# Kernel optimization log

Measured on AMD Instinct MI355X. Metric: run time of the kernel, lower is better.

The kernel has to match this reference:

```python
import jax, jax.numpy as jnp
import numpy as np

D_MODEL = 1024
N_HEADS = 16
HEAD_DIM = D_MODEL // N_HEADS
D_FF = 4096
B, S = 2, 2048
EPS = 1e-6
NEG = -1e9


def setup_inputs() -> dict:
    key = jax.random.key(0)
    ks = jax.random.split(key, 16)
    sd = 1.0 / np.sqrt(D_MODEL)
    sf = 1.0 / np.sqrt(D_FF)
    inp = {
        "x": jax.random.normal(ks[0], (B, S, D_MODEL), jnp.float32),
        # causal mask, broadcastable over batch and heads
        "mask": jnp.tril(jnp.ones((S, S), jnp.bool_))[None, None, :, :],
        # attention projections, torch Linear layout [out, in]
        "Wq": jax.random.normal(ks[1], (D_MODEL, D_MODEL), jnp.float32) * sd,
        "bq": jnp.zeros((D_MODEL,), jnp.float32),
        "Wk": jax.random.normal(ks[2], (D_MODEL, D_MODEL), jnp.float32) * sd,
        "bk": jnp.zeros((D_MODEL,), jnp.float32),
        "Wv": jax.random.normal(ks[3], (D_MODEL, D_MODEL), jnp.float32) * sd,
        "bv": jnp.zeros((D_MODEL,), jnp.float32),
        "Wo": jax.random.normal(ks[4], (D_MODEL, D_MODEL), jnp.float32) * sd,
        "bo": jnp.zeros((D_MODEL,), jnp.float32),
        # layer norms
        "ln1_g": jnp.ones((D_MODEL,), jnp.float32),
        "ln1_b": jnp.zeros((D_MODEL,), jnp.float32),
        "ln2_g": jnp.ones((D_MODEL,), jnp.float32),
        "ln2_b": jnp.zeros((D_MODEL,), jnp.float32),
        # FFN
        "W1": jax.random.normal(ks[5], (D_FF, D_MODEL), jnp.float32) * sd,
        "b1": jnp.zeros((D_FF,), jnp.float32),
        "W2": jax.random.normal(ks[6], (D_MODEL, D_FF), jnp.float32) * sf,
        "b2": jnp.zeros((D_MODEL,), jnp.float32),
    }
    return inp


def _layer_norm(x, g, b):
    mu = jnp.mean(x, axis=-1, keepdims=True)
    var = jnp.var(x, axis=-1, keepdims=True)
    return (x - mu) * jax.lax.rsqrt(var + EPS) * g + b


def _linear(x, W, b):
    return jnp.einsum('...i,oi->...o', x, W) + b


def _attention(x, mask, Wq, bq, Wk, bk, Wv, bv, Wo, bo):
    Bsz, Sq, _ = x.shape
    q = _linear(x, Wq, bq).reshape(Bsz, Sq, N_HEADS, HEAD_DIM)
    k = _linear(x, Wk, bk).reshape(Bsz, Sq, N_HEADS, HEAD_DIM)
    v = _linear(x, Wv, bv).reshape(Bsz, Sq, N_HEADS, HEAD_DIM)
    # [B,H,S,S]
    scores = jnp.einsum('bqhd,bkhd->bhqk', q, k) / np.sqrt(HEAD_DIM)
    scores = jnp.where(mask, scores, NEG)
    weights = jax.nn.softmax(scores, axis=-1)
    ctx = jnp.einsum('bhqk,bkhd->bqhd', weights, v).reshape(Bsz, Sq, D_MODEL)
    return _linear(ctx, Wo, bo)


def reference(x, mask, Wq, bq, Wk, bk, Wv, bv, Wo, bo,
              ln1_g, ln1_b, ln2_g, ln2_b, W1, b1, W2, b2):
    # pre-LN attention block (dropout = identity at inference)
    h = _layer_norm(x, ln1_g, ln1_b)
    x = x + _attention(h, mask, Wq, bq, Wk, bk, Wv, bv, Wo, bo)
    # pre-LN FFN block
    h = _layer_norm(x, ln2_g, ln2_b)
    h = jax.nn.gelu(_linear(h, W1, b1), approximate=False)
    x = x + _linear(h, W2, b2)
    return x
```

## Files before the change

kernel.cpp:

```cpp
#include <hip/hip_runtime.h>
#include <hip/hip_bf16.h>
#include <cstdint>
#include <cstddef>

typedef unsigned short u16;
typedef __bf16 bf16x8 __attribute__((ext_vector_type(8)));
typedef float f32x4 __attribute__((ext_vector_type(4)));

#define D_MODEL 1024
#define D_FF    4096
#define BATCH   2
#define SEQ     2048
#define NH      16
#define HD      64
#define ROWS    (BATCH*SEQ)
#define QKVS    3072

__device__ __forceinline__ u16 f2bf(float f) {
    union { float f; uint32_t u; } v; v.f = f;
    uint32_t u = v.u;
    u += 0x7FFF + ((u >> 16) & 1);
    return (u16)(u >> 16);
}

__device__ __forceinline__ uint32_t cvtpk_bf16(float lo, float hi) {
    uint32_t r;
    asm("v_cvt_pk_bf16_f32 %0, %1, %2" : "=v"(r) : "v"(lo), "v"(hi));
    return r;
}

__device__ __forceinline__ bf16x8 ldg8(const u16* p) {
    return *reinterpret_cast<const bf16x8*>(p);
}

__device__ __forceinline__ f32x4 mfma16(bf16x8 a, bf16x8 b, f32x4 c) {
    return __builtin_amdgcn_mfma_f32_16x16x32_bf16(a, b, c, 0, 0, 0);
}

__device__ __forceinline__ void gld_lds16(const void* g, void* l) {
    __builtin_amdgcn_global_load_lds(
        (const __attribute__((address_space(1))) void*)g,
        (__attribute__((address_space(3))) void*)l, 16, 0, 0);
}

__device__ __forceinline__ float gelu_f(float x) {
    float u = fmaf(0.044715f * x, x * x, x);
    float z = fminf(-2.3022036f * u, 126.0f);
    float e = __builtin_amdgcn_exp2f(z);
    return x / (1.0f + e);
}

struct alignas(8) U16x4 { u16 x, y, z, w; };

__global__ void cvt_all(const float* __restrict__ s0, const float* __restrict__ s1,
                        const float* __restrict__ s2, const float* __restrict__ s3,
                        const float* __restrict__ s4, const float* __restrict__ s5,
                        u16* __restrict__ out)
{
    const size_t MM1 = 1 << 20;
    size_t i = ((size_t)blockIdx.x * 256 + threadIdx.x) * 4;
    const float* src; size_t off;
    if      (i <     MM1) { src = s0; off = i; }
    else if (i < 2 * MM1) { src = s1; off = i - MM1; }
    else if (i < 3 * MM1) { src = s2; off = i - 2 * MM1; }
    else if (i < 4 * MM1) { src = s3; off = i - 3 * MM1; }
    else if (i < 8 * MM1) { src = s4; off = i - 4 * MM1; }
    else                  { src = s5; off = i - 8 * MM1; }
    float4 f = *reinterpret_cast<const float4*>(src + off);
    U16x4 o{ f2bf(f.x), f2bf(f.y), f2bf(f.z), f2bf(f.w) };
    *reinterpret_cast<U16x4*>(out + i) = o;
}

__global__ __launch_bounds__(256) void ln_bf16(
    const float* __restrict__ x, const float* __restrict__ g,
    const float* __restrict__ b, u16* __restrict__ out)
{
    int row = blockIdx.x;
    const float* xr = x + (size_t)row * D_MODEL;
    int t = threadIdx.x;
    float4 v = *reinterpret_cast<const float4*>(xr + t * 4);
    float s = v.x + v.y + v.z + v.w;
    float q = v.x*v.x + v.y*v.y + v.z*v.z + v.w*v.w;
    #pragma unroll
    for (int off = 1; off < 64; off <<= 1) {
        s += __shfl_xor(s, off);
        q += __shfl_xor(q, off);
    }
    __shared__ float red[8];
    if ((t & 63) == 0) { red[(t >> 6) * 2] = s; red[(t >> 6) * 2 + 1] = q; }
    __syncthreads();
    float sum = red[0] + red[2] + red[4] + red[6];
    float sq  = red[1] + red[3] + red[5] + red[7];
    float mu  = sum * (1.0f / D_MODEL);
    float var = sq * (1.0f / D_MODEL) - mu * mu;
    float rstd = rsqrtf(var + 1e-6f);
    float4 gg = *reinterpret_cast<const float4*>(g + t * 4);
    float4 bb = *reinterpret_cast<const float4*>(b + t * 4);
    U16x4 o{ f2bf((v.x - mu) * rstd * gg.x + bb.x),
             f2bf((v.y - mu) * rstd * gg.y + bb.y),
             f2bf((v.z - mu) * rstd * gg.z + bb.z),
             f2bf((v.w - mu) * rstd * gg.w + bb.w) };
    *reinterpret_cast<U16x4*>(out + (size_t)row * D_MODEL + t * 4) = o;
}

#define EPI_BF16   0
#define EPI_RESF32 1
#define EPI_GELU   2
#define EPI_PART   3

template<int EPI>
__global__ __launch_bounds__(512, 1) void gemm256(
    const u16* __restrict__ A, const u16* __restrict__ B,
    const float* __restrict__ bias, const float* __restrict__ res,
    u16* __restrict__ outb, float* __restrict__ outf,
    int M, int N, int K)
{
    __shared__ u16 As[2][256 * 64];
    __shared__ u16 Bs[2][256 * 64];
    const int t = threadIdx.x;
    const int lane = t & 63, w = t >> 6;
    const int lr = lane & 15, lg = lane >> 4;
    const int wr = w >> 2, wc = w & 3;

    const int gw  = N >> 8;
    const int nwg = gridDim.x;
    const int cpx = nwg >> 3;
    const int swz = ((int)blockIdx.x & 7) * cpx + ((int)blockIdx.x >> 3);
    const int by = swz / gw, bx = swz % gw;
    const int brow = by * 256, bcol = bx * 256;

    const u16* Ag = A + (size_t)brow * K;
    const u16* Bg = B + (size_t)bcol * K;

    f32x4 acc[8][4] = {};
    const int NT = K >> 6;

    auto stageAll = [&](int buf, int kt) {
        #pragma unroll
        for (int c = 0; c < 8; ++c) {
            const u16* g = (c < 4) ? Ag : Bg;
            u16* l = (c < 4) ? As[buf] : Bs[buf];
            int cc = c & 3;
            int row = cc * 64 + (t >> 3);
            int sg = (t & 7) ^ (row & 7);
            gld_lds16(g + (size_t)row * K + kt * 64 + sg * 8, l + cc * 4096 + t * 8);
        }
    };

    auto computeTile = [&](int buf) {
        const u16* la = As[buf];
        const u16* lb = Bs[buf];
        bf16x8 breg[4][2];
        #pragma unroll
        for (int ni = 0; ni < 4; ++ni) {
            int row = wc * 64 + ni * 16 + lr;
            const u16* bp = lb + row * 64;
            int key = row & 7;
            breg[ni][0] = ldg8(bp + ((0 + lg) ^ key) * 8);
            breg[ni][1] = ldg8(bp + ((4 + lg) ^ key) * 8);
        }
        #pragma unroll
        for (int mi = 0; mi < 8; ++mi) {
            int row = wr * 128 + mi * 16 + lr;
            const u16* ap = la + row * 64;
            int key = row & 7;
            bf16x8 a0 = ldg8(ap + ((0 + lg) ^ key) * 8);
            bf16x8 a1 = ldg8(ap + ((4 + lg) ^ key) * 8);
            __builtin_amdgcn_s_setprio(1);
            #pragma unroll
            for (int ni = 0; ni < 4; ++ni) {
                acc[mi][ni] = mfma16(a0, breg[ni][0], acc[mi][ni]);
                acc[mi][ni] = mfma16(a1, breg[ni][1], acc[mi][ni]);
            }
            __builtin_amdgcn_s_setprio(0);
        }
    };

    stageAll(0, 0);
    stageAll(1, 1);
    asm volatile("s_waitcnt vmcnt(8)" ::: "memory");
    __builtin_amdgcn_s_barrier();

    for (int kt = 0; kt < NT; ++kt) {
        computeTile(kt & 1);
        if (kt + 1 == NT) break;
        __builtin_amdgcn_s_barrier();
        if (kt + 2 < NT) {
            stageAll(kt & 1, kt + 2);
            asm volatile("s_waitcnt vmcnt(8)" ::: "memory");
        } else {
            asm volatile("s_waitcnt vmcnt(0)" ::: "memory");
        }
        __builtin_amdgcn_s_barrier();
    }

    #pragma unroll
    for (int mi = 0; mi < 8; ++mi) {
        int r0 = brow + wr * 128 + mi * 16 + lg * 4;
        #pragma unroll
        for (int ni = 0; ni < 4; ++ni) {
            int c = bcol + wc * 64 + ni * 16 + lr;
            float bv = bias[c];
            #pragma unroll
            for (int j = 0; j < 4; ++j) {
                float v = acc[mi][ni][j] + bv;
                size_t idx = (size_t)(r0 + j) * N + c;
                if constexpr (EPI == EPI_GELU) {
                    outb[idx] = f2bf(gelu_f(v));
                } else if constexpr (EPI == EPI_RESF32) {
                    outf[idx] = v + res[idx];
                } else {
                    outb[idx] = f2bf(v);
                }
            }
        }
    }
}

template<int EPI>
__global__ __launch_bounds__(256, 2) void gemm_bt(
    const u16* __restrict__ A, const u16* __restrict__ B,
    const float* __restrict__ bias, const float* __restrict__ res,
    u16* __restrict__ outb, float* __restrict__ outf,
    int M, int N, int K, int KS)
{
    __shared__ u16 As[2][128 * 64];
    __shared__ u16 Bs[2][128 * 64];
    const int t = threadIdx.x;
    const int lane = t & 63;
    const int w = t >> 6;
    const int lr = lane & 15, lg = lane >> 4;
    const int wrr = (w >> 1) * 64, wcc = (w & 1) * 64;
    const int brow = blockIdx.y * 128, bcol = blockIdx.x * 128;
    const int kz = blockIdx.z;
    const u16* Ag = A + (size_t)brow * KS + (size_t)kz * K;
    const u16* Bg = B + (size_t)bcol * KS + (size_t)kz * K;

    f32x4 acc[4][4] = {};

    const int NT = K >> 6;

    auto stage = [&](int buf, int kt) {
        const u16* ga = Ag + kt * 64;
        const u16* gb = Bg + kt * 64;
        u16* la = As[buf];
        u16* lb = Bs[buf];
        #pragma unroll
        for (int c = 0; c < 4; ++c) {
            int f = c * 256 + t;
            int row = f >> 3, slot = f & 7;
            int sg = slot ^ (row & 7);
            gld_lds16(ga + (size_t)row * KS + sg * 8, la + f * 8);
            gld_lds16(gb + (size_t)row * KS + sg * 8, lb + f * 8);
        }
    };

    auto compute = [&](int buf) {
        const u16* la = As[buf];
        const u16* lb = Bs[buf];
        bf16x8 af[4][2];
        #pragma unroll
        for (int mi = 0; mi < 4; ++mi) {
            int row = wrr + mi * 16 + lr;
            int base = row * 64;
            af[mi][0] = *reinterpret_cast<const bf16x8*>(la + base + ((0 + lg) ^ (row & 7)) * 8);
            af[mi][1] = *reinterpret_cast<const bf16x8*>(la + base + ((4 + lg) ^ (row & 7)) * 8);
        }
        __builtin_amdgcn_s_setprio(1);
        #pragma unroll
        for (int ni = 0; ni < 4; ++ni) {
            int row = wcc + ni * 16 + lr;
            int base = row * 64;
            bf16x8 b0 = *reinterpret_cast<const bf16x8*>(lb + base + ((0 + lg) ^ (row & 7)) * 8);
            bf16x8 b1 = *reinterpret_cast<const bf16x8*>(lb + base + ((4 + lg) ^ (row & 7)) * 8);
            #pragma unroll
            for (int mi = 0; mi < 4; ++mi) {
                acc[mi][ni] = mfma16(af[mi][0], b0, acc[mi][ni]);
                acc[mi][ni] = mfma16(af[mi][1], b1, acc[mi][ni]);
            }
        }
        __builtin_amdgcn_s_setprio(0);
    };

    stage(0, 0);
    if (NT > 1) {
        stage(1, 1);
        asm volatile("s_waitcnt vmcnt(8)" ::: "memory");
    } else {
        asm volatile("s_waitcnt vmcnt(0)" ::: "memory");
    }
    __builtin_amdgcn_s_barrier();

    for (int kt = 0; kt < NT; ++kt) {
        compute(kt & 1);
        if (kt + 1 == NT) break;
        __builtin_amdgcn_s_barrier();
        if (kt + 2 < NT) {
            stage(kt & 1, kt + 2);
            asm volatile("s_waitcnt vmcnt(8)" ::: "memory");
        } else {
            asm volatile("s_waitcnt vmcnt(0)" ::: "memory");
        }
        __builtin_amdgcn_s_barrier();
    }

    #pragma unroll
    for (int mi = 0; mi < 4; ++mi) {
        int r0 = brow + wrr + mi * 16 + lg * 4;
        #pragma unroll
        for (int ni = 0; ni < 4; ++ni) {
            int c = bcol + wcc + ni * 16 + lr;
            float bv = 0.f;
            if constexpr (EPI != EPI_PART) bv = bias[c];
            #pragma unroll
            for (int j = 0; j < 4; ++j) {
                float v = acc[mi][ni][j] + bv;
                size_t idx = (size_t)(r0 + j) * N + c;
                if constexpr (EPI == EPI_GELU) {
                    outb[idx] = f2bf(gelu_f(v));
                } else if constexpr (EPI == EPI_RESF32) {
                    outf[idx] = v + res[idx];
                } else if constexpr (EPI == EPI_PART) {
                    outf[idx + (size_t)kz * M * N] = v;
                } else {
                    outb[idx] = f2bf(v);
                }
            }
        }
    }
}

__global__ void ffn2_reduce(const float* __restrict__ p,
                            const float* __restrict__ b2,
                            const float* __restrict__ x2,
                            float* __restrict__ out)
{
    size_t i = ((size_t)blockIdx.x * 256 + threadIdx.x) * 4;
    float4 a0 = *reinterpret_cast<const float4*>(p + i);
    float4 a1 = *reinterpret_cast<const float4*>(p + (size_t)ROWS * D_MODEL + i);
    float4 r  = *reinterpret_cast<const float4*>(x2 + i);
    float4 bb = *reinterpret_cast<const float4*>(b2 + (i & (D_MODEL - 1)));
    float4 o;
    o.x = a0.x + a1.x + r.x + bb.x;
    o.y = a0.y + a1.y + r.y + bb.y;
    o.z = a0.z + a1.z + r.z + bb.z;
    o.w = a0.w + a1.w + r.w + bb.w;
    *reinterpret_cast<float4*>(out + i) = o;
}

__global__ __launch_bounds__(256) void vtrans(
    const u16* __restrict__ QKV, u16* __restrict__ VT)
{
    __shared__ u16 tile[64][72];
    const int st = blockIdx.x * 64;
    const int bh = blockIdx.y;
    const int b = bh >> 4, h = bh & 15;
    const int t = threadIdx.x;

    #pragma unroll
    for (int c = 0; c < 2; ++c) {
        int tok = c * 32 + (t >> 3);
        int d0 = (t & 7) * 8;
        bf16x8 v = ldg8(QKV + ((size_t)(b * SEQ + st + tok)) * QKVS + 2048 + h * HD + d0);
        *reinterpret_cast<bf16x8*>(&tile[tok][d0]) = v;
    }
    __syncthreads();
    u16* dst = VT + (size_t)bh * HD * SEQ + st;
    #pragma unroll
    for (int c = 0; c < 2; ++c) {
        int d = c * 32 + (t >> 3);
        int tok0 = (t & 7) * 8;
        u16 vals[8];
        #pragma unroll
        for (int i = 0; i < 8; ++i) vals[i] = tile[tok0 + i][d];
        *reinterpret_cast<bf16x8*>(dst + (size_t)d * SEQ + tok0) =
            *reinterpret_cast<const bf16x8*>(vals);
    }
}

#define QBLK  64
#define KVBLK 64

__global__ __launch_bounds__(256, 3) void attn7(
    const u16* __restrict__ QKV, const u16* __restrict__ VT,
    u16* __restrict__ O)
{
    __shared__ u16 Ks[2][64 * 64];
    __shared__ u16 Vs[2][64 * 64];
    __shared__ u16 Pl[4][16 * 72];

    const int i  = blockIdx.x;
    const int bh = blockIdx.y;
    const int b = bh >> 4, h = bh & 15;
    const int qta = 31 - i;
    const int qtb = i;
    const int q0a = qta * QBLK, q0b = qtb * QBLK;
    const int t = threadIdx.x;
    const int lane = t & 63, w = t >> 6;
    const int lr = lane & 15, lg = lane >> 4;

    const size_t rowbase = (size_t)b * SEQ;
    const u16* Qg = QKV + rowbase * QKVS + h * HD;
    const u16* Kg = Qg + 1024;
    const u16* Vg = VT + (size_t)bh * HD * SEQ;

    const u16* qpa = Qg + (size_t)(q0a + w * 16 + lr) * QKVS;
    const u16* qpb = Qg + (size_t)(q0b + w * 16 + lr) * QKVS;
    bf16x8 qa0 = ldg8(qpa + lg * 8), qa1 = ldg8(qpa + 32 + lg * 8);
    bf16x8 qb0 = ldg8(qpb + lg * 8), qb1 = ldg8(qpb + 32 + lg * 8);

    f32x4 oa[4] = {}, ob[4] = {};
    float lsa[4] = {}, lsb[4] = {};

    const int ntiles = qta + 1;
    u16* Pw = Pl[w];
    const float SC = 0.125f * 1.44269504089f;

    auto stage = [&](int buf, int tt) {
        const int kv0 = tt * KVBLK;
        #pragma unroll
        for (int c = 0; c < 2; ++c) {
            int f = c * 256 + t;
            int row = f >> 3, slot = f & 7;
            int sgk = slot ^ ((row >> 2) & 7);
            int sgv = slot ^ (row & 7);
            gld_lds16(Kg + (size_t)(kv0 + row) * QKVS + sgk * 8, Ks[buf] + f * 8);
            gld_lds16(Vg + (size_t)row * SEQ + kv0 + sgv * 8, Vs[buf] + f * 8);
        }
    };

    auto qtile = [&](bf16x8 qf0, bf16x8 qf1, f32x4* o, float* ls,
                     int q0, int kv0, bool diag, const u16* kb, const u16* vb) {
        f32x4 s[4] = {};
        __builtin_amdgcn_s_setprio(1);
        #pragma unroll
        for (int ni = 0; ni < 4; ++ni) {
            int row = lr * 4 + ni;
            const u16* base = kb + row * 64;
            int key = (row >> 2) & 7;
            bf16x8 k0 = *reinterpret_cast<const bf16x8*>(base + ((0 + lg) ^ key) * 8);
            bf16x8 k1 = *reinterpret_cast<const bf16x8*>(base + ((4 + lg) ^ key) * 8);
            s[ni] = mfma16(qf0, k0, s[ni]);
            s[ni] = mfma16(qf1, k1, s[ni]);
        }
        __builtin_amdgcn_s_setprio(0);

        #pragma unroll
        for (int j = 0; j < 4; ++j) {
            int qi = q0 + w * 16 + lg * 4 + j;
            float p0 = __builtin_amdgcn_exp2f(s[0][j] * SC);
            float p1 = __builtin_amdgcn_exp2f(s[1][j] * SC);
            float p2 = __builtin_amdgcn_exp2f(s[2][j] * SC);
            float p3 = __builtin_amdgcn_exp2f(s[3][j] * SC);
            if (diag) {
                int kvb = kv0 + lr * 4;
                p0 = (kvb     <= qi) ? p0 : 0.f;
                p1 = (kvb + 1 <= qi) ? p1 : 0.f;
                p2 = (kvb + 2 <= qi) ? p2 : 0.f;
                p3 = (kvb + 3 <= qi) ? p3 : 0.f;
            }
            ls[j] += (p0 + p1) + (p2 + p3);
            uint2 pk = make_uint2(cvtpk_bf16(p0, p1), cvtpk_bf16(p2, p3));
            *reinterpret_cast<uint2*>(&Pw[(lg * 4 + j) * 72 + lr * 4]) = pk;
        }

        bf16x8 pa0 = *reinterpret_cast<const bf16x8*>(Pw + lr * 72 + lg * 8);
        bf16x8 pa1 = *reinterpret_cast<const bf16x8*>(Pw + lr * 72 + 32 + lg * 8);
        __builtin_amdgcn_s_setprio(1);
        #pragma unroll
        for (int ni = 0; ni < 4; ++ni) {
            int row = ni * 16 + lr;
            const u16* base = vb + row * 64;
            bf16x8 v0 = *reinterpret_cast<const bf16x8*>(base + ((0 + lg) ^ (row & 7)) * 8);
            bf16x8 v1 = *reinterpret_cast<const bf16x8*>(base + ((4 + lg) ^ (row & 7)) * 8);
            o[ni] = mfma16(pa0, v0, o[ni]);
            o[ni] = mfma16(pa1, v1, o[ni]);
        }
        __builtin_amdgcn_s_setprio(0);
    };

    stage(0, 0);
    stage(1, 1);
    asm volatile("s_waitcnt vmcnt(4)" ::: "memory");
    __builtin_amdgcn_s_barrier();

    for (int tt = 0; tt < ntiles; ++tt) {
        const int buf = tt & 1;
        const int kv0 = tt * KVBLK;
        const u16* kb = Ks[buf];
        const u16* vb = Vs[buf];

        qtile(qa0, qa1, oa, lsa, q0a, kv0, tt == qta, kb, vb);
        if (tt <= qtb)
            qtile(qb0, qb1, ob, lsb, q0b, kv0, tt == qtb, kb, vb);

        if (tt + 1 == ntiles) break;
        __builtin_amdgcn_s_barrier();
        if (tt + 2 < ntiles) {
            stage(buf, tt + 2);
            asm volatile("s_waitcnt vmcnt(4)" ::: "memory");
        } else {
            asm volatile("s_waitcnt vmcnt(0)" ::: "memory");
        }
        __builtin_amdgcn_s_barrier();
    }

    #pragma unroll
    for (int j = 0; j < 4; ++j) {
        float va = lsa[j], vb2 = lsb[j];
        va += __shfl_xor(va, 1); vb2 += __shfl_xor(vb2, 1);
        va += __shfl_xor(va, 2); vb2 += __shfl_xor(vb2, 2);
        va += __shfl_xor(va, 4); vb2 += __shfl_xor(vb2, 4);
        va += __shfl_xor(va, 8); vb2 += __shfl_xor(vb2, 8);
        lsa[j] = va; lsb[j] = vb2;
    }

    u16* Oa = O + (rowbase + q0a + w * 16) * D_MODEL + h * HD;
    u16* Ob = O + (rowbase + q0b + w * 16) * D_MODEL + h * HD;
    #pragma unroll
    for (int j = 0; j < 4; ++j) {
        float inva = 1.0f / lsa[j];
        float invb = 1.0f / lsb[j];
        int r = (lg * 4 + j) * D_MODEL;
        #pragma unroll
        for (int ni = 0; ni < 4; ++ni) {
            Oa[r + ni * 16 + lr] = f2bf(oa[ni][j] * inva);
            Ob[r + ni * 16 + lr] = f2bf(ob[ni][j] * invb);
        }
    }
}

extern "C" void kernel_launch(void* const* d_in, const int* in_sizes, int n_in,
                              void* d_out, int out_size, void* d_ws, size_t ws_size,
                              hipStream_t stream)
{
    (void)in_sizes; (void)n_in; (void)out_size; (void)ws_size;
    const float* x   = (const float*)d_in[0];
    const float* Wq  = (const float*)d_in[2];
    const float* bq  = (const float*)d_in[3];
    const float* Wk  = (const float*)d_in[4];
    const float* bk  = (const float*)d_in[5];
    const float* Wv  = (const float*)d_in[6];
    const float* bv  = (const float*)d_in[7];
    const float* Wo  = (const float*)d_in[8];
    const float* bo  = (const float*)d_in[9];
    const float* g1  = (const float*)d_in[10];
    const float* be1 = (const float*)d_in[11];
    const float* g2  = (const float*)d_in[12];
    const float* be2 = (const float*)d_in[13];
    const float* W1  = (const float*)d_in[14];
    const float* b1  = (const float*)d_in[15];
    const float* W2  = (const float*)d_in[16];
    const float* b2  = (const float*)d_in[17];
    float* out = (float*)d_out;

    const size_t MM = 1 << 20;
    u16* Wqkv_b = (u16*)d_ws;
    u16* Wo_b = Wqkv_b + 3 * MM;
    u16* W1_b = Wo_b + MM;
    u16* W2_b = W1_b + 4 * MM;
    u16* hbuf = W2_b + 4 * MM;
    u16* QKVb = hbuf + 4 * MM;
    u16* ctx  = QKVb + 12 * MM;
    u16* ffn1 = ctx + 4 * MM;
    float* x2 = (float*)(ffn1 + 16 * MM);
    float* bqkv = (float*)(x2 + 4 * MM);
    u16* VTb = hbuf;
    float* fpart = (float*)QKVb;

    cvt_all<<<12 * MM / 1024, 256, 0, stream>>>(Wq, Wk, Wv, Wo, W1, W2, Wqkv_b);

    hipMemcpyAsync(bqkv,        bq, D_MODEL * sizeof(float), hipMemcpyDeviceToDevice, stream);
    hipMemcpyAsync(bqkv + 1024, bk, D_MODEL * sizeof(float), hipMemcpyDeviceToDevice, stream);
    hipMemcpyAsync(bqkv + 2048, bv, D_MODEL * sizeof(float), hipMemcpyDeviceToDevice, stream);

    ln_bf16<<<ROWS, 256, 0, stream>>>(x, g1, be1, hbuf);

    dim3 gqkv(QKVS / 128, ROWS / 128);
    gemm_bt<EPI_BF16><<<gqkv, 256, 0, stream>>>(hbuf, Wqkv_b, bqkv, nullptr,
                                                QKVb, nullptr, ROWS, QKVS, 1024, 1024);

    vtrans<<<dim3(SEQ / 64, BATCH * NH), 256, 0, stream>>>(QKVb, VTb);

    dim3 ga(SEQ / QBLK / 2, BATCH * NH);
    attn7<<<ga, 256, 0, stream>>>(QKVb, VTb, ctx);

    dim3 gq(D_MODEL / 128, ROWS / 128);
    gemm_bt<EPI_RESF32><<<gq, 256, 0, stream>>>(ctx, Wo_b, bo, x, nullptr, x2,
                                                ROWS, D_MODEL, 1024, 1024);

    ln_bf16<<<ROWS, 256, 0, stream>>>(x2, g2, be2, hbuf);

    gemm256<EPI_GELU><<<(ROWS / 256) * (D_FF / 256), 512, 0, stream>>>(
        hbuf, W1_b, b1, nullptr, ffn1, nullptr, ROWS, D_FF, D_MODEL);

    dim3 gf2(D_MODEL / 128, ROWS / 128, 2);
    gemm_bt<EPI_PART><<<gf2, 256, 0, stream>>>(ffn1, W2_b, nullptr, nullptr,
                                               nullptr, fpart, ROWS, D_MODEL, 2048, 4096);
    ffn2_reduce<<<(ROWS * D_MODEL) / 1024, 256, 0, stream>>>(fpart, b2, x2, out);
}
```

Measured before the change: 242.2 us.

## Replace 256-tile double-buffered FFN1 GEMM with 128-tile single-buffer kernel, reuse for QKV

Replaces the 256x256, 512-thread double-buffered GEMM with a 128x128, 256-thread single-buffered kernel that allows four blocks per CU. The new kernel is used for both the FFN1 (GELU) GEMM and the QKV projection, which previously ran through gemm_bt. The aim is higher occupancy and more blocks to fill the CUs. In exchange, each block loses explicit load/compute pipelining and gets less data reuse per tile.

```diff
diff --git a/kernel.cpp b/kernel.cpp
--- a/kernel.cpp
+++ b/kernel.cpp
@@ -109,97 +109,69 @@
 #define EPI_PART   3
 
 template<int EPI>
-__global__ __launch_bounds__(512, 1) void gemm256(
+__global__ __launch_bounds__(256, 4) void gemm97(
     const u16* __restrict__ A, const u16* __restrict__ B,
     const float* __restrict__ bias, const float* __restrict__ res,
     u16* __restrict__ outb, float* __restrict__ outf,
-    int M, int N, int K)
-{
-    __shared__ u16 As[2][256 * 64];
-    __shared__ u16 Bs[2][256 * 64];
+    int M, int N, int K, int KS)
+{
+    __shared__ u16 As[128 * 64];
+    __shared__ u16 Bs[128 * 64];
     const int t = threadIdx.x;
     const int lane = t & 63, w = t >> 6;
     const int lr = lane & 15, lg = lane >> 4;
-    const int wr = w >> 2, wc = w & 3;
-
-    const int gw  = N >> 8;
-    const int nwg = gridDim.x;
-    const int cpx = nwg >> 3;
-    const int swz = ((int)blockIdx.x & 7) * cpx + ((int)blockIdx.x >> 3);
-    const int by = swz / gw, bx = swz % gw;
-    const int brow = by * 256, bcol = bx * 256;
-
-    const u16* Ag = A + (size_t)brow * K;
-    const u16* Bg = B + (size_t)bcol * K;
-
-    f32x4 acc[8][4] = {};
+    const int wrr = (w >> 1) * 64, wcc = (w & 1) * 64;
+    const int brow = blockIdx.y * 128, bcol = blockIdx.x * 128;
+    const u16* Ag = A + (size_t)brow * KS;
+    const u16* Bg = B + (size_t)bcol * KS;
+
+    f32x4 acc[4][4] = {};
     const int NT = K >> 6;
 
-    auto stageAll = [&](int buf, int kt) {
-        #pragma unroll
-        for (int c = 0; c < 8; ++c) {
-            const u16* g = (c < 4) ? Ag : Bg;
-            u16* l = (c < 4) ? As[buf] : Bs[buf];
-            int cc = c & 3;
-            int row = cc * 64 + (t >> 3);
-            int sg = (t & 7) ^ (row & 7);
-            gld_lds16(g + (size_t)row * K + kt * 64 + sg * 8, l + cc * 4096 + t * 8);
-        }
-    };
-
-    auto computeTile = [&](int buf) {
-        const u16* la = As[buf];
-        const u16* lb = Bs[buf];
-        bf16x8 breg[4][2];
-        #pragma unroll
-        for (int ni = 0; ni < 4; ++ni) {
-            int row = wc * 64 + ni * 16 + lr;
-            const u16* bp = lb + row * 64;
+    for (int kt = 0; kt < NT; ++kt) {
+        #pragma unroll
+        for (int c = 0; c < 4; ++c) {
+            int f = c * 256 + t;
+            int row = f >> 3, slot = f & 7;
+            int sg = slot ^ (row & 7);
+            gld_lds16(Ag + (size_t)row * KS + kt * 64 + sg * 8, As + f * 8);
+            gld_lds16(Bg + (size_t)row * KS + kt * 64 + sg * 8, Bs + f * 8);
+        }
+        __syncthreads();
+
+        bf16x8 af[4][2];
+        #pragma unroll
+        for (int mi = 0; mi < 4; ++mi) {
+            int row = wrr + mi * 16 + lr;
+            const u16* bp = As + row * 64;
             int key = row & 7;
-            breg[ni][0] = ldg8(bp + ((0 + lg) ^ key) * 8);
-            breg[ni][1] = ldg8(bp + ((4 + lg) ^ key) * 8);
-        }
-        #pragma unroll
-        for (int mi = 0; mi < 8; ++mi) {
-            int row = wr * 128 + mi * 16 + lr;
-            const u16* ap = la + row * 64;
+            af[mi][0] = ldg8(bp + ((0 + lg) ^ key) * 8);
+            af[mi][1] = ldg8(bp + ((4 + lg) ^ key) * 8);
+        }
+        __builtin_amdgcn_s_setprio(1);
+        #pragma unroll
+        for (int ni = 0; ni < 4; ++ni) {
+            int row = wcc + ni * 16 + lr;
+            const u16* bp = Bs + row * 64;
             int key = row & 7;
-            bf16x8 a0 = ldg8(ap + ((0 + lg) ^ key) * 8);
-            bf16x8 a1 = ldg8(ap + ((4 + lg) ^ key) * 8);
-            __builtin_amdgcn_s_setprio(1);
+            bf16x8 b0 = ldg8(bp + ((0 + lg) ^ key) * 8);
+            bf16x8 b1 = ldg8(bp + ((4 + lg) ^ key) * 8);
             #pragma unroll
-            for (int ni = 0; ni < 4; ++ni) {
-                acc[mi][ni] = mfma16(a0, breg[ni][0], acc[mi][ni]);
-                acc[mi][ni] = mfma16(a1, breg[ni][1], acc[mi][ni]);
+            for (int mi = 0; mi < 4; ++mi) {
+                acc[mi][ni] = mfma16(af[mi][0], b0, acc[mi][ni]);
+                acc[mi][ni] = mfma16(af[mi][1], b1, acc[mi][ni]);
             }
-            __builtin_amdgcn_s_setprio(0);
-        }
-    };
-
-    stageAll(0, 0);
-    stageAll(1, 1);
-    asm volatile("s_waitcnt vmcnt(8)" ::: "memory");
-    __builtin_amdgcn_s_barrier();
-
-    for (int kt = 0; kt < NT; ++kt) {
-        computeTile(kt & 1);
-        if (kt + 1 == NT) break;
-        __builtin_amdgcn_s_barrier();
-        if (kt + 2 < NT) {
-            stageAll(kt & 1, kt + 2);
-            asm volatile("s_waitcnt vmcnt(8)" ::: "memory");
-        } else {
-            asm volatile("s_waitcnt vmcnt(0)" ::: "memory");
-        }
-        __builtin_amdgcn_s_barrier();
-    }
-
-    #pragma unroll
-    for (int mi = 0; mi < 8; ++mi) {
-        int r0 = brow + wr * 128 + mi * 16 + lg * 4;
-        #pragma unroll
-        for (int ni = 0; ni < 4; ++ni) {
-            int c = bcol + wc * 64 + ni * 16 + lr;
+        }
+        __builtin_amdgcn_s_setprio(0);
+        __syncthreads();
+    }
+
+    #pragma unroll
+    for (int mi = 0; mi < 4; ++mi) {
+        int r0 = brow + wrr + mi * 16 + lg * 4;
+        #pragma unroll
+        for (int ni = 0; ni < 4; ++ni) {
+            int c = bcol + wcc + ni * 16 + lr;
             float bv = bias[c];
             #pragma unroll
             for (int j = 0; j < 4; ++j) {
@@ -577,8 +549,8 @@
     ln_bf16<<<ROWS, 256, 0, stream>>>(x, g1, be1, hbuf);
 
     dim3 gqkv(QKVS / 128, ROWS / 128);
-    gemm_bt<EPI_BF16><<<gqkv, 256, 0, stream>>>(hbuf, Wqkv_b, bqkv, nullptr,
-                                                QKVb, nullptr, ROWS, QKVS, 1024, 1024);
+    gemm97<EPI_BF16><<<gqkv, 256, 0, stream>>>(hbuf, Wqkv_b, bqkv, nullptr,
+                                               QKVb, nullptr, ROWS, QKVS, 1024, 1024);
 
     vtrans<<<dim3(SEQ / 64, BATCH * NH), 256, 0, stream>>>(QKVb, VTb);
 
@@ -591,8 +563,9 @@
 
     ln_bf16<<<ROWS, 256, 0, stream>>>(x2, g2, be2, hbuf);
 
-    gemm256<EPI_GELU><<<(ROWS / 256) * (D_FF / 256), 512, 0, stream>>>(
-        hbuf, W1_b, b1, nullptr, ffn1, nullptr, ROWS, D_FF, D_MODEL);
+    dim3 gf1(D_FF / 128, ROWS / 128);
+    gemm97<EPI_GELU><<<gf1, 256, 0, stream>>>(hbuf, W1_b, b1, nullptr, ffn1, nullptr,
+                                              ROWS, D_FF, 1024, 1024);
 
     dim3 gf2(D_MODEL / 128, ROWS / 128, 2);
     gemm_bt<EPI_PART><<<gf2, 256, 0, stream>>>(ffn1, W2_b, nullptr, nullptr,
```

After: 238.0 us. No clear change (-1.7%).
